# Kernel optimization log

Hardware: AMD Instinct MI355X
Metric: run time of the kernel (lower is better)

## Reference

```python
import jax, jax.numpy as jnp
import numpy as np

N = 50000   # nodes
E = 600000  # edges (avg degree ~12)
R = 8       # num_relations = 2 * n_speakers**2, n_speakers=2
B = 32      # num_bases = args.batch_size
GD, H1, H2 = 128, 128, 128


def setup_inputs() -> dict:
    key = jax.random.key(0)
    ks = jax.random.split(key, 16)
    w = lambda k, shape: jax.random.normal(k, shape, jnp.float32) * 0.05
    return {
        "node_features": jax.random.normal(ks[0], (N, GD), jnp.float32),
        "edge_index": jax.random.randint(ks[1], (2, E), 0, N),
        "edge_norm": jax.random.uniform(ks[2], (E,), jnp.float32),
        "edge_type": jax.random.randint(ks[3], (E,), 0, R),
        "basis": w(ks[4], (B, GD, H1)),
        "comp": w(ks[5], (R, B)),
        "root": w(ks[6], (GD, H1)),
        "bias1": jnp.zeros((H1,), jnp.float32),
        "w_key": w(ks[7], (H1, H2)),
        "b_key": jnp.zeros((H2,), jnp.float32),
        "w_query": w(ks[8], (H1, H2)),
        "b_query": jnp.zeros((H2,), jnp.float32),
        "w_value": w(ks[9], (H1, H2)),
        "b_value": jnp.zeros((H2,), jnp.float32),
        "w_skip": w(ks[10], (H1, H2)),
        "b_skip": jnp.zeros((H2,), jnp.float32),
    }


def reference(node_features, edge_index, edge_norm, edge_type, basis, comp,
              root, bias1, w_key, b_key, w_query, b_query, w_value, b_value,
              w_skip, b_skip):
    n = node_features.shape[0]
    r = comp.shape[0]
    src, dst = edge_index[0], edge_index[1]

    # ---- RGCNConv (basis decomposition, per-relation mean aggregation) ----
    W = jnp.einsum('rb,bio->rio', comp, basis)            # [R, GD, H1]
    xW = jnp.einsum('ni,rio->rno', node_features, W)      # [R, N, H1]
    msg = xW[edge_type, src]                              # [E, H1]
    seg = edge_type * n + dst                             # combined (relation, dst) segment id
    agg = jax.ops.segment_sum(msg, seg, num_segments=r * n).reshape(r, n, -1)
    cnt = jax.ops.segment_sum(jnp.ones(msg.shape[0], jnp.float32), seg,
                              num_segments=r * n).reshape(r, n, 1)
    h = (agg / jnp.maximum(cnt, 1.0)).sum(0) + node_features @ root + bias1

    # ---- ResGatedGraphConv: sigmoid(k_i + q_j) * v_j, sum-aggregated + skip ----
    k = h @ w_key + b_key
    q = h @ w_query + b_query
    v = h @ w_value + b_value
    m = jax.nn.sigmoid(k[dst] + q[src]) * v[src]          # [E, H2]
    out = jax.ops.segment_sum(m, dst, num_segments=n) + h @ w_skip + b_skip
    return out
```

## Files before the change

kernel.cpp:

```cpp
#include <hip/hip_runtime.h>
#include <stdint.h>

#define GD 128
#define H1 128
#define H2 128
#define NBASES 32
#define NREL 8
#define KA 1152

typedef __attribute__((ext_vector_type(8))) short bf16x8;
typedef __attribute__((ext_vector_type(4))) float f32x4;

static inline size_t align256(size_t x){ return (x + 255) & ~(size_t)255; }

__device__ __forceinline__ float bf2f(uint32_t u16){
  union { uint32_t u; float f; } c; c.u = (u16 & 0xffffu) << 16; return c.f;
}
__device__ __forceinline__ unsigned short f2bf(float f){
  union { float f; uint32_t u; } c; c.f = f;
  uint32_t u = c.u;
  u += 0x7fffu + ((u >> 16) & 1u);
  return (unsigned short)(u >> 16);
}
__device__ __forceinline__ uint32_t pkbf(float a, float b){
  union { float f; uint32_t u; } ca, cb; ca.f = a; cb.f = b;
  return __builtin_amdgcn_perm(cb.u + 0x8000u, ca.u + 0x8000u, 0x07060302u);
}

__device__ __forceinline__ void async_copy16(void* lds_dst, const void* gsrc){
  __builtin_amdgcn_global_load_lds(
      (const __attribute__((address_space(1))) uint32_t*)gsrc,
      (__attribute__((address_space(3))) uint32_t*)lds_dst, 16, 0, 0);
}

__global__ void k_prep(const float* __restrict__ comp, const float* __restrict__ basis,
                       const float* __restrict__ root, unsigned short* __restrict__ Bht,
                       const float* __restrict__ wk, const float* __restrict__ wq,
                       const float* __restrict__ wv, const float* __restrict__ wsk,
                       const float* __restrict__ bk, const float* __restrict__ bq,
                       const float* __restrict__ bv, const float* __restrict__ bs,
                       unsigned short* __restrict__ B2t, float* __restrict__ Bb,
                       const float4* __restrict__ x, uint2* __restrict__ xout, int cnt4,
                       uint32_t* __restrict__ xpadz, int npadz,
                       const int* __restrict__ edst, const int* __restrict__ etyp,
                       int* __restrict__ cnt, int E, int n){
  const float LOG2E = 1.4426950408889634f;
  int b = blockIdx.x, t = threadIdx.x;
  if (b < 128){
    int i = b;
    int o = t & 127, rh = t >> 7;
    float bv[NBASES];
    #pragma unroll
    for (int bb = 0; bb < NBASES; ++bb)
      bv[bb] = basis[((size_t)bb*GD + i)*H1 + o];
    #pragma unroll
    for (int rr = 0; rr < 4; ++rr){
      int r = rh*4 + rr;
      float acc = 0.f;
      #pragma unroll
      for (int bb = 0; bb < NBASES; ++bb)
        acc += comp[r*NBASES + bb] * bv[bb];
      Bht[(size_t)o*KA + r*128 + i] = f2bf(acc);
    }
    if (rh == 1) Bht[(size_t)o*KA + 1024 + i] = f2bf(root[(size_t)i*H1 + o]);
  } else if (b < 128 + 256){
    int idx = (b - 128)*256 + t;
    int c = idx / H1, k = idx % H1;
    const float* w = (c < 128) ? wk : (c < 256) ? wq : (c < 384) ? wv : wsk;
    float val = w[(size_t)k*H2 + (c & 127)];
    if (c < 256) val *= LOG2E;
    B2t[idx] = f2bf(val);
    if (idx < 512){
      const float* bia = (idx < 128) ? bk : (idx < 256) ? bq : (idx < 384) ? bv : bs;
      float bval = bia[idx & 127];
      if (idx < 256) bval *= LOG2E;
      Bb[idx] = bval;
    }
  } else {
    int cb = b - (128 + 256);
    int ncastb = (cnt4 + 1023) >> 10;
    if (cb < ncastb){
      int base = cb*1024 + t;
      #pragma unroll
      for (int u = 0; u < 4; ++u){
        int i = base + u*256;
        if (i < cnt4){
          float4 v = x[i];
          uint2 o; o.x = pkbf(v.x, v.y); o.y = pkbf(v.z, v.w);
          xout[i] = o;
        }
      }
    } else if (cb < ncastb + 12){
      int i = (cb - ncastb)*256 + t;
      if (i < npadz) xpadz[i] = 0u;
    } else {
      int e = (cb - ncastb - 12)*256 + t;
      if (e < E) atomicAdd(&cnt[etyp[e]*n + edst[e]], 1);
    }
  }
}

__global__ void k_scanA(const int* __restrict__ deg, int* __restrict__ off,
                        int* __restrict__ btot, int len){
  __shared__ int wsum[16];
  int t = threadIdx.x, lane = t & 63, w = t >> 6;
  int i0 = blockIdx.x*8192 + t*8;
  int v[8];
  if (i0 + 7 < len){
    int4 va = *(const int4*)(deg + i0);
    int4 vb = *(const int4*)(deg + i0 + 4);
    v[0]=va.x; v[1]=va.y; v[2]=va.z; v[3]=va.w;
    v[4]=vb.x; v[5]=vb.y; v[6]=vb.z; v[7]=vb.w;
  } else {
    #pragma unroll
    for (int u = 0; u < 8; ++u) v[u] = (i0+u < len) ? deg[i0+u] : 0;
  }
  int s[8]; s[0] = v[0];
  #pragma unroll
  for (int u = 1; u < 8; ++u) s[u] = s[u-1] + v[u];
  int x = s[7];
  #pragma unroll
  for (int d = 1; d < 64; d <<= 1){
    int u = __shfl_up(x, d, 64);
    if (lane >= d) x += u;
  }
  if (lane == 63) wsum[w] = x;
  __syncthreads();
  if (t < 16){
    int y = wsum[t];
    #pragma unroll
    for (int d = 1; d < 16; d <<= 1){
      int u = __shfl_up(y, d, 16);
      if (t >= d) y += u;
    }
    wsum[t] = y;
  }
  __syncthreads();
  int woff = (w > 0) ? wsum[w-1] : 0;
  int excl = woff + x - s[7];
  #pragma unroll
  for (int u = 0; u < 8; ++u)
    if (i0+u < len) off[i0+u] = excl + s[u] - v[u];
  if (t == 0) btot[blockIdx.x] = wsum[15];
}

__global__ void k_scanB(const int* __restrict__ btot, int* __restrict__ off,
                        int* __restrict__ cursor, int len, int sentinel){
  int t = threadIdx.x, bid = blockIdx.x;
  int add = 0;
  for (int j = 0; j < bid; ++j) add += btot[j];
  int i0 = bid*8192 + t*8;
  #pragma unroll
  for (int u = 0; u < 8; ++u){
    int i = i0 + u;
    if (i < len){ int val = off[i] + add; off[i] = val; cursor[i] = val; }
  }
  if (bid == 0 && t == 0) off[len] = sentinel;
}

__global__ void k_scatter_rd(const int* __restrict__ src, const int* __restrict__ dst,
                             const int* __restrict__ typ, int* __restrict__ cursor,
                             int* __restrict__ pk, int E, int n){
  int e = blockIdx.x*blockDim.x + threadIdx.x;
  if (e >= E) return;
  int pos = atomicAdd(&cursor[typ[e]*n + dst[e]], 1);
  pk[pos] = src[e];
}

__global__ void k_agg(const int* __restrict__ off_rd, const int* __restrict__ pk_rd,
                      const uint32_t* __restrict__ x32, unsigned short* __restrict__ A2,
                      int n, int npad){
  int wid = blockIdx.x*(blockDim.x >> 6) + (threadIdx.x >> 6);
  int lane = threadIdx.x & 63;
  if (wid >= npad) return;
  uint32_t* arow = (uint32_t*)(A2 + (size_t)wid*1024);
  if (wid >= n){
    #pragma unroll
    for (int u = 0; u < 8; ++u) arow[u*64 + lane] = 0u;
    return;
  }
  int r8 = lane & 7;
  int o_r = off_rd[(size_t)r8*n + wid];
  int e_r = off_rd[(size_t)r8*n + wid + 1];
  int c_r = e_r - o_r;
  float ic_r = (c_r > 0) ? __builtin_amdgcn_rcpf((float)c_r) : 0.f;
  int c0_ = __builtin_amdgcn_readlane(c_r, 0), c1_ = __builtin_amdgcn_readlane(c_r, 1);
  int c2_ = __builtin_amdgcn_readlane(c_r, 2), c3_ = __builtin_amdgcn_readlane(c_r, 3);
  int c4_ = __builtin_amdgcn_readlane(c_r, 4), c5_ = __builtin_amdgcn_readlane(c_r, 5);
  int c6_ = __builtin_amdgcn_readlane(c_r, 6), c7_ = __builtin_amdgcn_readlane(c_r, 7);
  int o0_ = __builtin_amdgcn_readlane(o_r, 0), o1_ = __builtin_amdgcn_readlane(o_r, 1);
  int o2_ = __builtin_amdgcn_readlane(o_r, 2), o3_ = __builtin_amdgcn_readlane(o_r, 3);
  int o4_ = __builtin_amdgcn_readlane(o_r, 4), o5_ = __builtin_amdgcn_readlane(o_r, 5);
  int o6_ = __builtin_amdgcn_readlane(o_r, 6), o7_ = __builtin_amdgcn_readlane(o_r, 7);
  int p1 = c0_, p2 = p1 + c1_, p3 = p2 + c2_, p4 = p3 + c3_;
  int p5 = p4 + c4_, p6 = p5 + c5_, p7 = p6 + c6_, dg = p7 + c7_;

  int cr = 0;
  float a0 = 0.f, a1 = 0.f;

#define FLUSH(RK)                                                               \
  {                                                                             \
    float ic = __int_as_float(__builtin_amdgcn_readlane(__float_as_int(ic_r), cr)); \
    arow[cr*64 + lane] = pkbf(a0*ic, a1*ic);                                    \
    for (int q = cr + 1; q < (RK); ++q) arow[q*64 + lane] = 0u;                 \
    cr = (RK); a0 = 0.f; a1 = 0.f;                                              \
  }

  for (int jb = 0; jb < dg; jb += 64){
    int i = jb + lane;
    int adj = o0_, rel = 0;
    adj = (i >= p1) ? (o1_ - p1) : adj;  rel += (i >= p1);
    adj = (i >= p2) ? (o2_ - p2) : adj;  rel += (i >= p2);
    adj = (i >= p3) ? (o3_ - p3) : adj;  rel += (i >= p3);
    adj = (i >= p4) ? (o4_ - p4) : adj;  rel += (i >= p4);
    adj = (i >= p5) ? (o5_ - p5) : adj;  rel += (i >= p5);
    adj = (i >= p6) ? (o6_ - p6) : adj;  rel += (i >= p6);
    adj = (i >= p7) ? (o7_ - p7) : adj;  rel += (i >= p7);
    int m = dg - jb; if (m > 64) m = 64;
    int pj = (lane < m) ? pk_rd[adj + i] : 0;
    int jj = 0;
    for (; jj + 8 <= m; jj += 8){
      uint32_t g[8];
      #pragma unroll
      for (int k = 0; k < 8; ++k){
        int sN = __builtin_amdgcn_readlane(pj, jj + k);
        g[k] = x32[(size_t)(uint32_t)sN*64 + lane];
      }
      #pragma unroll
      for (int k = 0; k < 8; ++k){
        int rk = __builtin_amdgcn_readlane(rel, jj + k);
        if (rk != cr) FLUSH(rk);
        a0 += bf2f(g[k]); a1 += bf2f(g[k] >> 16);
      }
    }
    for (; jj < m; jj += 4){
      int lim = m - 1;
      uint32_t g[4];
      #pragma unroll
      for (int k = 0; k < 4; ++k){
        int tt = jj + k; if (tt > lim) tt = lim;
        int sN = __builtin_amdgcn_readlane(pj, tt);
        g[k] = x32[(size_t)(uint32_t)sN*64 + lane];
      }
      #pragma unroll
      for (int k = 0; k < 4; ++k){
        int tt = jj + k;
        if (tt < m){
          int rk = __builtin_amdgcn_readlane(rel, tt);
          if (rk != cr) FLUSH(rk);
          a0 += bf2f(g[k]); a1 += bf2f(g[k] >> 16);
        }
      }
    }
  }
  FLUSH(8)
#undef FLUSH
}

__launch_bounds__(256)
__global__ void k_hqkv(const unsigned short* __restrict__ A, const unsigned short* __restrict__ xb,
                       const unsigned short* __restrict__ Bt,
                       const unsigned short* __restrict__ B2,
                       const float* __restrict__ bias1, const float* __restrict__ Bb,
                       unsigned short* __restrict__ kqv, unsigned short* __restrict__ skipb){
  __shared__ char lds[45568];
  int t = threadIdx.x, lane = t & 63, wave = t >> 6;
  int row0 = blockIdx.x * 64;
  int mrow = lane & 15, quad = lane >> 4;
  int s = (mrow >> 1) & 3;
  int colsw = (((t & 3) ^ ((t >> 3) & 3)) << 3);

  const unsigned short* Asrc = A  + (size_t)(row0 + (t >> 2))*1024 + colsw;
  const unsigned short* Xsrc = xb + (size_t)(row0 + (t >> 2))*GD   + colsw;
  const unsigned short* Bsrc = Bt + (size_t)(t >> 2)*KA + colsw;
  char* ldsB  = lds + 4096;
  char* htile = lds + 12288;
  char* eb    = lds + 28672;

  int aoff = mrow*64 + ((quad ^ s) << 4);
  int boff = 4096 + (wave*32 + mrow)*64 + ((quad ^ s) << 4);
  int axor = (mrow & 7) << 4;

  f32x4 acc[4][2];
  #pragma unroll
  for (int i = 0; i < 4; ++i)
    #pragma unroll
    for (int j = 0; j < 2; ++j) acc[i][j] = (f32x4){0.f,0.f,0.f,0.f};

  for (int kt = 0; kt < KA; kt += 32){
    const unsigned short* ap = (kt < 1024) ? (Asrc + kt) : (Xsrc + (kt - 1024));
    __syncthreads();
    async_copy16(lds  + wave*1024, ap);
    async_copy16(ldsB + wave*1024, Bsrc + kt);
    async_copy16(ldsB + 4096 + wave*1024, Bsrc + (size_t)64*KA + kt);
    __syncthreads();
    bf16x8 af[4], bf[2];
    #pragma unroll
    for (int i = 0; i < 4; ++i) af[i] = *(const bf16x8*)(lds + aoff + i*1024);
    #pragma unroll
    for (int j = 0; j < 2; ++j) bf[j] = *(const bf16x8*)(lds + boff + j*1024);
    #pragma unroll
    for (int i = 0; i < 4; ++i)
      #pragma unroll
      for (int j = 0; j < 2; ++j)
        acc[i][j] = __builtin_amdgcn_mfma_f32_16x16x32_bf16(af[i], bf[j], acc[i][j], 0, 0, 0);
  }
  {
    float bc1[2];
    #pragma unroll
    for (int j = 0; j < 2; ++j) bc1[j] = bias1[wave*32 + j*16 + mrow];
    #pragma unroll
    for (int j = 0; j < 2; ++j){
      int col = wave*32 + j*16 + mrow;
      #pragma unroll
      for (int i = 0; i < 4; ++i)
        #pragma unroll
        for (int rg = 0; rg < 4; ++rg){
          int row = i*16 + quad*4 + rg;
          *(unsigned short*)(htile + row*256 + ((col*2) ^ ((row & 7) << 4)))
              = f2bf(acc[i][j][rg] + bc1[j]);
        }
    }
  }
  __syncthreads();

  for (int c0 = 0; c0 < 4; ++c0){
    #pragma unroll
    for (int i = 0; i < 4; ++i)
      #pragma unroll
      for (int j = 0; j < 2; ++j) acc[i][j] = (f32x4){0.f,0.f,0.f,0.f};
    const unsigned short* B2src = B2 + (size_t)(c0*128 + (t >> 2))*H1 + colsw;
    for (int kt = 0; kt < 128; kt += 32){
      __syncthreads();
      async_copy16(ldsB + wave*1024, B2src + kt);
      async_copy16(ldsB + 4096 + wave*1024, B2src + (size_t)64*H1 + kt);
      __syncthreads();
      bf16x8 af[4], bf[2];
      #pragma unroll
      for (int i = 0; i < 4; ++i)
        af[i] = *(const bf16x8*)(htile + (i*16 + mrow)*256 + (((kt + quad*8)*2) ^ axor));
      #pragma unroll
      for (int j = 0; j < 2; ++j) bf[j] = *(const bf16x8*)(lds + boff + j*1024);
      #pragma unroll
      for (int i = 0; i < 4; ++i)
        #pragma unroll
        for (int j = 0; j < 2; ++j)
          acc[i][j] = __builtin_amdgcn_mfma_f32_16x16x32_bf16(af[i], bf[j], acc[i][j], 0, 0, 0);
    }
    float bc2[2];
    #pragma unroll
    for (int j = 0; j < 2; ++j) bc2[j] = Bb[c0*128 + wave*32 + j*16 + mrow];
    #pragma unroll
    for (int j = 0; j < 2; ++j){
      int col = wave*32 + j*16 + mrow;
      #pragma unroll
      for (int i = 0; i < 4; ++i)
        #pragma unroll
        for (int rg = 0; rg < 4; ++rg){
          int rl = i*16 + quad*4 + rg;
          *(unsigned short*)(eb + rl*264 + col*2) = f2bf(acc[i][j][rg] + bc2[j]);
        }
    }
    __syncthreads();
    uint32_t vv[16];
    #pragma unroll
    for (int u = 0; u < 8; ++u)
      *(uint2*)&vv[u*2] = *(const uint2*)(eb + lane*264 + wave*64 + u*8);
    unsigned short* dstb; size_t ldu;
    if (c0 < 3){ dstb = kqv + c0*128; ldu = 384; } else { dstb = skipb; ldu = 128; }
    unsigned short* gp = dstb + (size_t)(row0 + lane)*ldu + wave*32;
    #pragma unroll
    for (int u = 0; u < 4; ++u)
      *(uint4*)(gp + u*8) = *(const uint4*)&vv[u*4];
    __syncthreads();
  }
}

__global__ void k_edge2(const int* __restrict__ off_rd, const int* __restrict__ pk_rd,
                        const unsigned short* __restrict__ kqv,
                        const unsigned short* __restrict__ skipb,
                        float* __restrict__ out, int n){
  int wid = blockIdx.x*(blockDim.x >> 6) + (threadIdx.x >> 6);
  int lane = threadIdx.x & 63;
  if (wid >= n) return;
  const uint32_t* kv32 = (const uint32_t*)kqv;
  int r = lane & 7;
  int o_r = off_rd[(size_t)r*n + wid];
  int e_r = off_rd[(size_t)r*n + wid + 1];
  int c_r = e_r - o_r;
  int c0_ = __builtin_amdgcn_readlane(c_r, 0), c1_ = __builtin_amdgcn_readlane(c_r, 1);
  int c2_ = __builtin_amdgcn_readlane(c_r, 2), c3_ = __builtin_amdgcn_readlane(c_r, 3);
  int c4_ = __builtin_amdgcn_readlane(c_r, 4), c5_ = __builtin_amdgcn_readlane(c_r, 5);
  int c6_ = __builtin_amdgcn_readlane(c_r, 6), c7_ = __builtin_amdgcn_readlane(c_r, 7);
  int o0_ = __builtin_amdgcn_readlane(o_r, 0), o1_ = __builtin_amdgcn_readlane(o_r, 1);
  int o2_ = __builtin_amdgcn_readlane(o_r, 2), o3_ = __builtin_amdgcn_readlane(o_r, 3);
  int o4_ = __builtin_amdgcn_readlane(o_r, 4), o5_ = __builtin_amdgcn_readlane(o_r, 5);
  int o6_ = __builtin_amdgcn_readlane(o_r, 6), o7_ = __builtin_amdgcn_readlane(o_r, 7);
  int p1 = c0_, p2 = p1 + c1_, p3 = p2 + c2_, p4 = p3 + c3_;
  int p5 = p4 + c4_, p6 = p5 + c5_, p7 = p6 + c6_, dg = p7 + c7_;

  uint32_t ku = kv32[(size_t)wid*192 + lane];
  float k0 = bf2f(ku), k1 = bf2f(ku >> 16);
  float a0 = 0.f, a1 = 0.f;
  for (int jb = 0; jb < dg; jb += 64){
    int i = jb + lane;
    int adj = o0_;
    adj = (i >= p1) ? (o1_ - p1) : adj;
    adj = (i >= p2) ? (o2_ - p2) : adj;
    adj = (i >= p3) ? (o3_ - p3) : adj;
    adj = (i >= p4) ? (o4_ - p4) : adj;
    adj = (i >= p5) ? (o5_ - p5) : adj;
    adj = (i >= p6) ? (o6_ - p6) : adj;
    adj = (i >= p7) ? (o7_ - p7) : adj;
    int m = dg - jb; if (m > 64) m = 64;
    int pj = (lane < m) ? pk_rd[adj + i] : 0;
    int jj = 0;
    for (; jj + 8 <= m; jj += 8){
      uint32_t qg[8], vg[8];
      #pragma unroll
      for (int k = 0; k < 8; ++k){
        int s = __builtin_amdgcn_readlane(pj, jj + k);
        const uint32_t* rowp = kv32 + (size_t)s*192 + lane;
        qg[k] = rowp[64];
        vg[k] = rowp[128];
      }
      #pragma unroll
      for (int k = 0; k < 8; ++k){
        float qq0 = bf2f(qg[k]), qq1 = bf2f(qg[k] >> 16);
        float vv0 = bf2f(vg[k]), vv1 = bf2f(vg[k] >> 16);
        float g0 = __builtin_amdgcn_rcpf(1.f + __builtin_amdgcn_exp2f(-(k0 + qq0)));
        float g1 = __builtin_amdgcn_rcpf(1.f + __builtin_amdgcn_exp2f(-(k1 + qq1)));
        a0 += g0*vv0; a1 += g1*vv1;
      }
    }
    for (; jj + 4 <= m; jj += 4){
      uint32_t qg[4], vg[4];
      #pragma unroll
      for (int k = 0; k < 4; ++k){
        int s = __builtin_amdgcn_readlane(pj, jj + k);
        const uint32_t* rowp = kv32 + (size_t)s*192 + lane;
        qg[k] = rowp[64];
        vg[k] = rowp[128];
      }
      #pragma unroll
      for (int k = 0; k < 4; ++k){
        float qq0 = bf2f(qg[k]), qq1 = bf2f(qg[k] >> 16);
        float vv0 = bf2f(vg[k]), vv1 = bf2f(vg[k] >> 16);
        float g0 = __builtin_amdgcn_rcpf(1.f + __builtin_amdgcn_exp2f(-(k0 + qq0)));
        float g1 = __builtin_amdgcn_rcpf(1.f + __builtin_amdgcn_exp2f(-(k1 + qq1)));
        a0 += g0*vv0; a1 += g1*vv1;
      }
    }
    for (; jj < m; ++jj){
      int s = __builtin_amdgcn_readlane(pj, jj);
      const uint32_t* rowp = kv32 + (size_t)s*192 + lane;
      uint32_t qg = rowp[64], vg = rowp[128];
      float qq0 = bf2f(qg), qq1 = bf2f(qg >> 16);
      float vv0 = bf2f(vg), vv1 = bf2f(vg >> 16);
      float g0 = __builtin_amdgcn_rcpf(1.f + __builtin_amdgcn_exp2f(-(k0 + qq0)));
      float g1 = __builtin_amdgcn_rcpf(1.f + __builtin_amdgcn_exp2f(-(k1 + qq1)));
      a0 += g0*vv0; a1 += g1*vv1;
    }
  }
  uint32_t sk = ((const uint32_t*)skipb)[(size_t)wid*64 + lane];
  float2 cur; cur.x = a0 + bf2f(sk); cur.y = a1 + bf2f(sk >> 16);
  ((float2*)(out + (size_t)wid*H2))[lane] = cur;
}

extern "C" void kernel_launch(void* const* d_in, const int* in_sizes, int n_in,
                              void* d_out, int out_size, void* d_ws, size_t ws_size,
                              hipStream_t stream){
  const float* x     = (const float*)d_in[0];
  const int*   eidx  = (const int*)  d_in[1];
  const int*   etype = (const int*)  d_in[3];
  const float* basis = (const float*)d_in[4];
  const float* comp  = (const float*)d_in[5];
  const float* root  = (const float*)d_in[6];
  const float* bias1 = (const float*)d_in[7];
  const float* wk    = (const float*)d_in[8];
  const float* bk    = (const float*)d_in[9];
  const float* wq    = (const float*)d_in[10];
  const float* bq    = (const float*)d_in[11];
  const float* wv    = (const float*)d_in[12];
  const float* bv    = (const float*)d_in[13];
  const float* wsk   = (const float*)d_in[14];
  const float* bs    = (const float*)d_in[15];
  const int n = in_sizes[0] / GD;
  const int E = in_sizes[3];
  const int npad = (n + 127) & ~127;
  const int* esrc = eidx;
  const int* edst = eidx + E;
  float* out = (float*)d_out;

  char* w = (char*)d_ws;
  size_t off = 0;
  unsigned short* xbf  = (unsigned short*)(w + off); off = align256(off + (size_t)npad*GD*2);
  unsigned short* A2   = (unsigned short*)(w + off); off = align256(off + (size_t)npad*1024*2);
  unsigned short* Bht  = (unsigned short*)(w + off); off = align256(off + (size_t)KA*H1*2);
  unsigned short* B2t  = (unsigned short*)(w + off); off = align256(off + (size_t)512*H1*2);
  float* Bb            = (float*)(w + off);          off = align256(off + 512*4);
  unsigned short* kqv  = (unsigned short*)(w + off); off = align256(off + (size_t)npad*384*2);
  unsigned short* skipb= (unsigned short*)(w + off); off = align256(off + (size_t)npad*H2*2);
  int* cnt_rd          = (int*)(w + off);            off = align256(off + (size_t)(8*n+4)*4);
  int* off_rd          = (int*)(w + off);            off = align256(off + (size_t)(8*n+1)*4);
  int* cur_rd          = (int*)(w + off);            off = align256(off + (size_t)8*n*4);
  int* btot_rd         = (int*)(w + off);            off = align256(off + 64*4);
  int* pk_rd           = (int*)(w + off);            off = align256(off + (size_t)E*4);

  const int nblk_rd = (8*n + 8191) / 8192;
  const int cnt4 = n*GD/4;
  const int ncastb = (cnt4 + 1023)/1024;
  const int histb  = (E + 255)/256;
  const int npadz  = (npad - n)*GD/2;

  hipMemsetAsync(cnt_rd, 0, (size_t)8*n*4, stream);

  k_prep<<<128 + 256 + ncastb + 12 + histb, 256, 0, stream>>>(
      comp, basis, root, Bht, wk, wq, wv, wsk, bk, bq, bv, bs, B2t, Bb,
      (const float4*)x, (uint2*)xbf, cnt4,
      (uint32_t*)(xbf + (size_t)n*GD), npadz,
      edst, etype, cnt_rd, E, n);
  k_scanA<<<nblk_rd, 1024, 0, stream>>>(cnt_rd, off_rd, btot_rd, 8*n);
  k_scanB<<<nblk_rd, 1024, 0, stream>>>(btot_rd, off_rd, cur_rd, 8*n, E);
  k_scatter_rd<<<(E + 255)/256, 256, 0, stream>>>(esrc, edst, etype, cur_rd, pk_rd, E, n);
  k_agg<<<(npad + 3)/4, 256, 0, stream>>>(off_rd, pk_rd, (const uint32_t*)xbf, A2, n, npad);
  k_hqkv<<<npad/64, 256, 0, stream>>>(A2, xbf, Bht, B2t, bias1, Bb, kqv, skipb);
  k_edge2<<<(n + 3)/4, 256, 0, stream>>>(off_rd, pk_rd, kqv, skipb, out, n);
}
```

Before: 338.9 us.

## Double-buffer LDS staging in k_hqkv GEMM loops to overlap loads with MFMA

Both GEMM phases of the fused h/kqv kernel now use two LDS buffers. The async copy for the next k-step is issued before the current step's MFMAs, which drops one of the two barriers per iteration. The second-phase loops over the four output chunks are flattened into a single 16-step pipelined loop. This is meant to hide global-to-LDS latency, at the cost of slightly more LDS per block, which may lower occupancy.

After: 334.9 us. No clear change (-1.2%).

```diff
diff --git a/kernel.cpp b/kernel.cpp
--- a/kernel.cpp
+++ b/kernel.cpp
@@ -263,7 +263,7 @@
                        const unsigned short* __restrict__ B2,
                        const float* __restrict__ bias1, const float* __restrict__ Bb,
                        unsigned short* __restrict__ kqv, unsigned short* __restrict__ skipb){
-  __shared__ char lds[45568];
+  __shared__ char lds[49664];
   int t = threadIdx.x, lane = t & 63, wave = t >> 6;
   int row0 = blockIdx.x * 64;
   int mrow = lane & 15, quad = lane >> 4;
@@ -273,12 +273,14 @@
   const unsigned short* Asrc = A  + (size_t)(row0 + (t >> 2))*1024 + colsw;
   const unsigned short* Xsrc = xb + (size_t)(row0 + (t >> 2))*GD   + colsw;
   const unsigned short* Bsrc = Bt + (size_t)(t >> 2)*KA + colsw;
-  char* ldsB  = lds + 4096;
-  char* htile = lds + 12288;
-  char* eb    = lds + 28672;
+  const unsigned short* B2src = B2 + (size_t)(t >> 2)*H1 + colsw;
+  char* Bstg  = lds;
+  char* htile = lds + 16384;
+  char* Astg  = lds + 32768;
+  char* eb    = lds + 32768;
 
   int aoff = mrow*64 + ((quad ^ s) << 4);
-  int boff = 4096 + (wave*32 + mrow)*64 + ((quad ^ s) << 4);
+  int boff = (wave*32 + mrow)*64 + ((quad ^ s) << 4);
   int axor = (mrow & 7) << 4;
 
   f32x4 acc[4][2];
@@ -287,24 +289,32 @@
     #pragma unroll
     for (int j = 0; j < 2; ++j) acc[i][j] = (f32x4){0.f,0.f,0.f,0.f};
 
-  for (int kt = 0; kt < KA; kt += 32){
-    const unsigned short* ap = (kt < 1024) ? (Asrc + kt) : (Xsrc + (kt - 1024));
-    __syncthreads();
-    async_copy16(lds  + wave*1024, ap);
-    async_copy16(ldsB + wave*1024, Bsrc + kt);
-    async_copy16(ldsB + 4096 + wave*1024, Bsrc + (size_t)64*KA + kt);
-    __syncthreads();
+#define STAGE1(B_, KT_)                                                           \
+  { const unsigned short* ap = ((KT_) < 1024) ? (Asrc + (KT_)) : (Xsrc + ((KT_) - 1024)); \
+    async_copy16(Astg + (B_)*4096 + wave*1024, ap);                               \
+    async_copy16(Bstg + (B_)*8192 + wave*1024, Bsrc + (KT_));                     \
+    async_copy16(Bstg + (B_)*8192 + 4096 + wave*1024, Bsrc + (size_t)64*KA + (KT_)); }
+
+  STAGE1(0, 0)
+  __syncthreads();
+  int b = 0;
+  for (int step = 0; step < 36; ++step){
+    if (step < 35) STAGE1(b^1, (step+1)*32)
     bf16x8 af[4], bf[2];
     #pragma unroll
-    for (int i = 0; i < 4; ++i) af[i] = *(const bf16x8*)(lds + aoff + i*1024);
-    #pragma unroll
-    for (int j = 0; j < 2; ++j) bf[j] = *(const bf16x8*)(lds + boff + j*1024);
+    for (int i = 0; i < 4; ++i) af[i] = *(const bf16x8*)(Astg + b*4096 + aoff + i*1024);
+    #pragma unroll
+    for (int j = 0; j < 2; ++j) bf[j] = *(const bf16x8*)(Bstg + b*8192 + boff + j*1024);
     #pragma unroll
     for (int i = 0; i < 4; ++i)
       #pragma unroll
       for (int j = 0; j < 2; ++j)
         acc[i][j] = __builtin_amdgcn_mfma_f32_16x16x32_bf16(af[i], bf[j], acc[i][j], 0, 0, 0);
-  }
+    __syncthreads();
+    b ^= 1;
+  }
+#undef STAGE1
+
   {
     float bc1[2];
     #pragma unroll
@@ -322,58 +332,69 @@
         }
     }
   }
+
+#define STAGE2(B_, C0_, KT_)                                                      \
+  { async_copy16(Bstg + (B_)*8192 + wave*1024, B2src + (C0_)*16384 + (KT_));      \
+    async_copy16(Bstg + (B_)*8192 + 4096 + wave*1024,                             \
+                 B2src + (C0_)*16384 + (size_t)64*H1 + (KT_)); }
+
+  STAGE2(b, 0, 0)
   __syncthreads();
 
-  for (int c0 = 0; c0 < 4; ++c0){
-    #pragma unroll
-    for (int i = 0; i < 4; ++i)
-      #pragma unroll
-      for (int j = 0; j < 2; ++j) acc[i][j] = (f32x4){0.f,0.f,0.f,0.f};
-    const unsigned short* B2src = B2 + (size_t)(c0*128 + (t >> 2))*H1 + colsw;
-    for (int kt = 0; kt < 128; kt += 32){
-      __syncthreads();
-      async_copy16(ldsB + wave*1024, B2src + kt);
-      async_copy16(ldsB + 4096 + wave*1024, B2src + (size_t)64*H1 + kt);
-      __syncthreads();
-      bf16x8 af[4], bf[2];
-      #pragma unroll
-      for (int i = 0; i < 4; ++i)
-        af[i] = *(const bf16x8*)(htile + (i*16 + mrow)*256 + (((kt + quad*8)*2) ^ axor));
-      #pragma unroll
-      for (int j = 0; j < 2; ++j) bf[j] = *(const bf16x8*)(lds + boff + j*1024);
+  for (int idx = 0; idx < 16; ++idx){
+    int ks = idx & 3;
+    if (idx < 15) STAGE2(b^1, (idx+1) >> 2, ((idx+1) & 3)*32)
+    if (ks == 0){
       #pragma unroll
       for (int i = 0; i < 4; ++i)
         #pragma unroll
-        for (int j = 0; j < 2; ++j)
-          acc[i][j] = __builtin_amdgcn_mfma_f32_16x16x32_bf16(af[i], bf[j], acc[i][j], 0, 0, 0);
-    }
-    float bc2[2];
-    #pragma unroll
-    for (int j = 0; j < 2; ++j) bc2[j] = Bb[c0*128 + wave*32 + j*16 + mrow];
-    #pragma unroll
-    for (int j = 0; j < 2; ++j){
-      int col = wave*32 + j*16 + mrow;
-      #pragma unroll
-      for (int i = 0; i < 4; ++i)
+        for (int j = 0; j < 2; ++j) acc[i][j] = (f32x4){0.f,0.f,0.f,0.f};
+    }
+    int kt = ks*32;
+    bf16x8 af[4], bf[2];
+    #pragma unroll
+    for (int i = 0; i < 4; ++i)
+      af[i] = *(const bf16x8*)(htile + (i*16 + mrow)*256 + (((kt + quad*8)*2) ^ axor));
+    #pragma unroll
+    for (int j = 0; j < 2; ++j) bf[j] = *(const bf16x8*)(Bstg + b*8192 + boff + j*1024);
+    #pragma unroll
+    for (int i = 0; i < 4; ++i)
+      #pragma unroll
+      for (int j = 0; j < 2; ++j)
+        acc[i][j] = __builtin_amdgcn_mfma_f32_16x16x32_bf16(af[i], bf[j], acc[i][j], 0, 0, 0);
+    if (ks == 3){
+      int c0 = idx >> 2;
+      float bc2[2];
+      #pragma unroll
+      for (int j = 0; j < 2; ++j) bc2[j] = Bb[c0*128 + wave*32 + j*16 + mrow];
+      #pragma unroll
+      for (int j = 0; j < 2; ++j){
+        int col = wave*32 + j*16 + mrow;
         #pragma unroll
-        for (int rg = 0; rg < 4; ++rg){
-          int rl = i*16 + quad*4 + rg;
-          *(unsigned short*)(eb + rl*264 + col*2) = f2bf(acc[i][j][rg] + bc2[j]);
-        }
-    }
-    __syncthreads();
-    uint32_t vv[16];
-    #pragma unroll
-    for (int u = 0; u < 8; ++u)
-      *(uint2*)&vv[u*2] = *(const uint2*)(eb + lane*264 + wave*64 + u*8);
-    unsigned short* dstb; size_t ldu;
-    if (c0 < 3){ dstb = kqv + c0*128; ldu = 384; } else { dstb = skipb; ldu = 128; }
-    unsigned short* gp = dstb + (size_t)(row0 + lane)*ldu + wave*32;
-    #pragma unroll
-    for (int u = 0; u < 4; ++u)
-      *(uint4*)(gp + u*8) = *(const uint4*)&vv[u*4];
-    __syncthreads();
-  }
+        for (int i = 0; i < 4; ++i)
+          #pragma unroll
+          for (int rg = 0; rg < 4; ++rg){
+            int rl = i*16 + quad*4 + rg;
+            *(unsigned short*)(eb + rl*264 + col*2) = f2bf(acc[i][j][rg] + bc2[j]);
+          }
+      }
+      __syncthreads();
+      uint32_t vv[16];
+      #pragma unroll
+      for (int u = 0; u < 8; ++u)
+        *(uint2*)&vv[u*2] = *(const uint2*)(eb + lane*264 + wave*64 + u*8);
+      unsigned short* dstb; size_t ldu;
+      if (c0 < 3){ dstb = kqv + c0*128; ldu = 384; } else { dstb = skipb; ldu = 128; }
+      unsigned short* gp = dstb + (size_t)(row0 + lane)*ldu + wave*32;
+      #pragma unroll
+      for (int u = 0; u < 4; ++u)
+        *(uint4*)(gp + u*8) = *(const uint4*)&vv[u*4];
+    } else {
+      __syncthreads();
+    }
+    b ^= 1;
+  }
+#undef STAGE2
 }
 
 __global__ void k_edge2(const int* __restrict__ off_rd, const int* __restrict__ pk_rd,
```
